# Optimization experiments

Hardware: AMD Instinct MI355X
Metric: run time of the kernel (lower is better)

## Reference

```python
import jax, jax.numpy as jnp
import numpy as np
from jax import lax

RADIUS = 4
SIGMA_1 = 5.0
SIGMA_2 = 1.0


def _gaussian_kernel_3d(radius, sigma):
    x = np.linspace(-radius, radius, 2 * radius + 1)
    xx, yy, zz = np.meshgrid(x, x, x)
    dist2 = xx ** 2 + yy ** 2 + zz ** 2
    k = np.exp(-dist2 / (2.0 * sigma ** 2)).astype(np.float32)
    return jnp.asarray(k)[None, None]  # [O=1, I=1, D, H, W]


def _conv3d_same(x, kernel, radius):
    # x: [B,1,D,H,W], kernel: [1,1,kd,kh,kw]
    pad = [(radius, radius)] * 3
    return lax.conv_general_dilated(
        x, kernel, window_strides=(1, 1, 1), padding=pad,
        dimension_numbers=('NCDHW', 'OIDHW', 'NCDHW'))


def setup_inputs() -> dict:
    key = jax.random.key(0)
    k1, k2 = jax.random.split(key)
    labels = jax.random.uniform(k1, (4, 1, 160, 160, 160), dtype=jnp.float32)
    inputs = jax.random.uniform(k2, (4, 1, 160, 160, 160), dtype=jnp.float32)
    return {"labels": labels, "inputs": inputs}


def reference(labels, inputs):
    kernel = _gaussian_kernel_3d(RADIUS, SIGMA_1)
    num_classes = 2
    p0 = labels[:, 0:1]  # [B,1,D,H,W]
    loss = jnp.float32(0.0)
    for k in range(num_classes):
        class_probs = p0 if k == 0 else 1.0 - p0
        class_mean = (jnp.mean(inputs * class_probs, axis=(2, 3, 4), keepdims=True)
                      / (jnp.mean(class_probs, axis=(2, 3, 4), keepdims=True) + 1e-5))
        diff = jnp.sum((inputs - class_mean) ** 2, axis=1, keepdims=True)  # [B,1,D,H,W]
        weights = jnp.exp(-(diff ** 2) / (SIGMA_2 ** 2))
        numerator = jnp.sum(class_probs * _conv3d_same(class_probs * weights, kernel, RADIUS))
        denominator = jnp.sum(class_probs * _conv3d_same(weights, kernel, RADIUS))
        # L1Loss(scalar, 0) == abs(scalar)
        loss = loss + jnp.abs(numerator / (denominator + 1e-6))
    return jnp.float32(num_classes) - loss
```

## Files before the change

### kernel.cpp

```cpp
#include <hip/hip_runtime.h>
#include <math.h>

#define NX   160
#define N2   25600
#define N3   4096000
#define NB   4

#define NTILES_XY 16000
#define TILES_PER_B 4000
#define NBLK_Z 800

#define SA_W 52
#define SB_W 36

__device__ __constant__ float G1[9] = {
    0.72614903f, 0.83527021f, 0.92311635f, 0.98019867f, 1.0f,
    0.98019867f, 0.92311635f, 0.83527021f, 0.72614903f};

#define ES_FULL 7.92946852f
__device__ __constant__ float ES_M[4] = {3.46473426f, 2.48453559f, 1.56141924f,
                                         0.72614903f};
__device__ inline float edge_sum(int i) {
    float s = ES_FULL;
    if (i < 4) s -= ES_M[i];
    if (i > NX - 5) s -= ES_M[NX - 1 - i];
    return s;
}

__device__ inline float4 f4_zero() { return make_float4(0.f, 0.f, 0.f, 0.f); }
__device__ inline float4 f4_axpy(float a, float4 b, float4 c) {
    return make_float4(c.x + a * b.x, c.y + a * b.y, c.z + a * b.z, c.w + a * b.w);
}

template <int NV>
__device__ inline void block_reduce_store(double* vals, double* dst) {
    __shared__ double red[4][NV];
    int lane = threadIdx.x & 63;
    int wave = threadIdx.x >> 6;
#pragma unroll
    for (int v = 0; v < NV; ++v) {
        double x = vals[v];
#pragma unroll
        for (int off = 32; off > 0; off >>= 1) x += __shfl_down(x, off, 64);
        if (lane == 0) red[wave][v] = x;
    }
    __syncthreads();
    if (threadIdx.x < NV) {
        int v = threadIdx.x;
        dst[v] = red[0][v] + red[1][v] + red[2][v] + red[3][v];
    }
}

__global__ __launch_bounds__(256) void conv_xy_kernel(
    const float* __restrict__ labels, const float* __restrict__ inputs,
    float* __restrict__ t, double* __restrict__ pS) {
    __shared__ float sA[40 * SA_W];
    __shared__ float sB[40 * SB_W];

    int bid = blockIdx.x;
    int tileX = bid % 5;
    int tileY = (bid / 5) % 5;
    int zb = bid / 25;
    int sliceOff = zb * N2;
    int x0 = tileX * 32, y0 = tileY * 32;
    int tid = threadIdx.x;

    for (int i = tid; i < 480; i += 256) {
        int row = i / 12, c = i % 12;
        int gx = x0 - 8 + 4 * c;
        int gy = y0 - 4 + row;
        float4 v = f4_zero();
        if (gy >= 0 && gy < NX && gx >= 0 && gx <= NX - 4)
            v = *(const float4*)&labels[sliceOff + gy * NX + gx];
        *(float4*)&sA[row * SA_W + 4 * c] = v;
    }
    __syncthreads();

    for (int i = tid; i < 320; i += 256) {
        int r = i >> 3, x4 = i & 7;
        const float* row = &sA[r * SA_W + 4 * x4];
        float4 a = *(const float4*)&row[4];
        float4 b = *(const float4*)&row[8];
        float4 c = *(const float4*)&row[12];
        float w[12] = {a.x, a.y, a.z, a.w, b.x, b.y, b.z, b.w,
                       c.x, c.y, c.z, c.w};
        float4 o = f4_zero();
#pragma unroll
        for (int d = 0; d < 9; ++d) {
            float g = G1[d];
            o.x += g * w[d];
            o.y += g * w[d + 1];
            o.z += g * w[d + 2];
            o.w += g * w[d + 3];
        }
        *(float4*)&sB[r * SB_W + 4 * x4] = o;
    }
    __syncthreads();

    int oy = tid >> 3, x4 = tid & 7;
    float4 acc = f4_zero();
#pragma unroll
    for (int d = 0; d < 9; ++d) {
        float4 v = *(const float4*)&sB[(oy + d) * SB_W + 4 * x4];
        acc = f4_axpy(G1[d], v, acc);
    }
    int gi = sliceOff + (y0 + oy) * NX + (x0 + 4 * x4);
    *(float4*)&t[gi] = acc;

    float4 p = *(const float4*)&sA[(oy + 4) * SA_W + 4 * x4 + 8];
    float4 in = *(const float4*)&inputs[gi];
    float sp = p.x + p.y + p.z + p.w;
    float sip = in.x * p.x + in.y * p.y + in.z * p.z + in.w * p.w;
    float si = in.x + in.y + in.z + in.w;
    double vals[3] = {(double)sp, (double)sip, (double)si};
    block_reduce_store<3>(vals, pS + 3 * bid);
}

__global__ __launch_bounds__(256) void reduce_S_kernel(
    const double* __restrict__ pS, double* __restrict__ S) {
    int b = blockIdx.x;
    double v0 = 0, v1 = 0, v2 = 0;
    for (int i = threadIdx.x; i < TILES_PER_B; i += 256) {
        const double* p = pS + 3 * (b * TILES_PER_B + i);
        v0 += p[0]; v1 += p[1]; v2 += p[2];
    }
    double vals[3] = {v0, v1, v2};
    block_reduce_store<3>(vals, S + 3 * b);
}

__global__ __launch_bounds__(256) void conv_z_reduce_kernel(
    const float* __restrict__ t, const float* __restrict__ labels,
    const float* __restrict__ inputs, const double* __restrict__ S,
    double* __restrict__ pZ) {
    int tidg = blockIdx.x * 256 + threadIdx.x;
    int x4 = tidg % 40;
    int r = tidg / 40;
    int y = r % NX;
    r /= NX;
    int zc = r % 8;
    int b = r / 8;

    double sp = S[3 * b + 0], sip = S[3 * b + 1], si = S[3 * b + 2];
    const double Nv = (double)N3;
    float m0 = (float)((sip / Nv) / (sp / Nv + 1e-5));
    float m1 = (float)(((si - sip) / Nv) / ((Nv - sp) / Nv + 1e-5));

    int x = x4 * 4;
    float ey = edge_sum(y);
    float cx[4] = {edge_sum(x) * ey, edge_sum(x + 1) * ey,
                   edge_sum(x + 2) * ey, edge_sum(x + 3) * ey};

    int z0 = zc * 20;
    int base = b * N3 + y * NX + x;

    float4 win[9];
#pragma unroll
    for (int d = 0; d < 9; ++d) {
        int z = z0 - 4 + d;
        win[d] = (z >= 0 && z < NX) ? *(const float4*)&t[base + z * N2]
                                    : f4_zero();
    }

    float n0 = 0.f, d0 = 0.f, n1 = 0.f, d1 = 0.f;
    for (int zb = 0; zb < 5; ++zb) {
        int z = z0 + 4 * zb;
        float4 tn[4], pv[4], iv[4];
#pragma unroll
        for (int j = 0; j < 4; ++j) {
            int zl = z + j + 5;
            tn[j] = (zl < NX) ? *(const float4*)&t[base + zl * N2] : f4_zero();
            int gi = base + (z + j) * N2;
            pv[j] = *(const float4*)&labels[gi];
            iv[j] = *(const float4*)&inputs[gi];
        }
#pragma unroll
        for (int j = 0; j < 4; ++j) {
            float4 c4 = f4_zero();
#pragma unroll
            for (int d = 0; d < 9; ++d) c4 = f4_axpy(G1[d], win[d], c4);
            float ez = edge_sum(z + j);
            float pc[4] = {pv[j].x, pv[j].y, pv[j].z, pv[j].w};
            float ic[4] = {iv[j].x, iv[j].y, iv[j].z, iv[j].w};
            float cc[4] = {c4.x, c4.y, c4.z, c4.w};
#pragma unroll
            for (int l = 0; l < 4; ++l) {
                float c1 = cx[l] * ez - cc[l];
                float df0 = ic[l] - m0; df0 *= df0;
                float w0 = __expf(-df0 * df0);
                float df1 = ic[l] - m1; df1 *= df1;
                float w1 = __expf(-df1 * df1);
                n0 += cc[l] * pc[l] * w0;
                d0 += cc[l] * w0;
                n1 += c1 * (1.f - pc[l]) * w1;
                d1 += c1 * w1;
            }
#pragma unroll
            for (int d = 0; d < 8; ++d) win[d] = win[d + 1];
            win[8] = tn[j];
        }
    }
    double vals[4] = {(double)n0, (double)d0, (double)n1, (double)d1};
    block_reduce_store<4>(vals, pZ + 4 * blockIdx.x);
}

__global__ __launch_bounds__(256) void finalize_kernel(
    const double* __restrict__ pZ, float* __restrict__ out) {
    double a0 = 0, a1 = 0, a2 = 0, a3 = 0;
    for (int i = threadIdx.x; i < NBLK_Z; i += 256) {
        const double* p = pZ + 4 * i;
        a0 += p[0]; a1 += p[1]; a2 += p[2]; a3 += p[3];
    }
    __shared__ double red[4][4];
    int lane = threadIdx.x & 63;
    int wave = threadIdx.x >> 6;
    double vals[4] = {a0, a1, a2, a3};
#pragma unroll
    for (int v = 0; v < 4; ++v) {
        double x = vals[v];
#pragma unroll
        for (int off = 32; off > 0; off >>= 1) x += __shfl_down(x, off, 64);
        if (lane == 0) red[wave][v] = x;
    }
    __syncthreads();
    if (threadIdx.x == 0) {
        double acc[4];
#pragma unroll
        for (int v = 0; v < 4; ++v)
            acc[v] = red[0][v] + red[1][v] + red[2][v] + red[3][v];
        double r0 = fabs(acc[0] / (acc[1] + 1e-6));
        double r1 = fabs(acc[2] / (acc[3] + 1e-6));
        out[0] = (float)(2.0 - r0 - r1);
    }
}

extern "C" void kernel_launch(void* const* d_in, const int* in_sizes, int n_in,
                              void* d_out, int out_size, void* d_ws, size_t ws_size,
                              hipStream_t stream) {
    const float* labels = (const float*)d_in[0];
    const float* inputs = (const float*)d_in[1];
    float* out = (float*)d_out;

    double* pS = (double*)d_ws;
    double* S  = (double*)((char*)d_ws + 384000);
    double* pZ = (double*)((char*)d_ws + 384096);
    float*  t  = (float*)((char*)d_ws + 524288);

    hipLaunchKernelGGL(conv_xy_kernel, dim3(NTILES_XY), dim3(256), 0, stream,
                       labels, inputs, t, pS);
    hipLaunchKernelGGL(reduce_S_kernel, dim3(NB), dim3(256), 0, stream, pS, S);
    hipLaunchKernelGGL(conv_z_reduce_kernel, dim3(NBLK_Z), dim3(256), 0, stream,
                       t, labels, inputs, S, pZ);
    hipLaunchKernelGGL(finalize_kernel, dim3(1), dim3(256), 0, stream, pZ, out);
}
```

Before: 206.4 us.

## Store XY-convolved intermediate in fp16 and fold reductions into last-block tickets

The intermediate XY-convolution buffer t is now written and read as fp16, halving its write and read traffic. The two small reduction kernels (per-batch sums and final scalar) are folded into their producers using an atomic ticket counter, so the last-finishing block does the final reduction, with counters cleared by a memset. The shared-memory staging of labels is removed in favour of direct global loads. The cost is fp16 rounding of the convolved values and an extra memset launch.

```diff
diff --git a/kernel.cpp b/kernel.cpp
--- a/kernel.cpp
+++ b/kernel.cpp
@@ -1,4 +1,5 @@
 #include <hip/hip_runtime.h>
+#include <hip/hip_fp16.h>
 #include <math.h>
 
 #define NX   160
@@ -10,7 +11,6 @@
 #define TILES_PER_B 4000
 #define NBLK_Z 800
 
-#define SA_W 52
 #define SB_W 36
 
 __device__ __constant__ float G1[9] = {
@@ -32,8 +32,17 @@
     return make_float4(c.x + a * b.x, c.y + a * b.y, c.z + a * b.z, c.w + a * b.w);
 }
 
+__device__ inline float4 load_t4(const __half* p) {
+    uint2 u = *(const uint2*)p;
+    __half2 a = *(const __half2*)&u.x;
+    __half2 b = *(const __half2*)&u.y;
+    float2 fa = __half22float2(a);
+    float2 fb = __half22float2(b);
+    return make_float4(fa.x, fa.y, fb.x, fb.y);
+}
+
 template <int NV>
-__device__ inline void block_reduce_store(double* vals, double* dst) {
+__device__ inline void block_reduce_to_t0(double* vals) {
     __shared__ double red[4][NV];
     int lane = threadIdx.x & 63;
     int wave = threadIdx.x >> 6;
@@ -45,16 +54,18 @@
         if (lane == 0) red[wave][v] = x;
     }
     __syncthreads();
-    if (threadIdx.x < NV) {
-        int v = threadIdx.x;
-        dst[v] = red[0][v] + red[1][v] + red[2][v] + red[3][v];
-    }
+    if (threadIdx.x == 0) {
+#pragma unroll
+        for (int v = 0; v < NV; ++v)
+            vals[v] = red[0][v] + red[1][v] + red[2][v] + red[3][v];
+    }
+    __syncthreads();
 }
 
 __global__ __launch_bounds__(256) void conv_xy_kernel(
     const float* __restrict__ labels, const float* __restrict__ inputs,
-    float* __restrict__ t, double* __restrict__ pS) {
-    __shared__ float sA[40 * SA_W];
+    __half* __restrict__ t, double* __restrict__ pS, double* __restrict__ S,
+    int* __restrict__ cnt) {
     __shared__ float sB[40 * SB_W];
 
     int bid = blockIdx.x;
@@ -65,25 +76,25 @@
     int x0 = tileX * 32, y0 = tileY * 32;
     int tid = threadIdx.x;
 
-    for (int i = tid; i < 480; i += 256) {
-        int row = i / 12, c = i % 12;
-        int gx = x0 - 8 + 4 * c;
-        int gy = y0 - 4 + row;
-        float4 v = f4_zero();
-        if (gy >= 0 && gy < NX && gx >= 0 && gx <= NX - 4)
-            v = *(const float4*)&labels[sliceOff + gy * NX + gx];
-        *(float4*)&sA[row * SA_W + 4 * c] = v;
-    }
-    __syncthreads();
-
     for (int i = tid; i < 320; i += 256) {
         int r = i >> 3, x4 = i & 7;
-        const float* row = &sA[r * SA_W + 4 * x4];
-        float4 a = *(const float4*)&row[4];
-        float4 b = *(const float4*)&row[8];
-        float4 c = *(const float4*)&row[12];
-        float w[12] = {a.x, a.y, a.z, a.w, b.x, b.y, b.z, b.w,
-                       c.x, c.y, c.z, c.w};
+        int gy = y0 + r - 4;
+        int gxf = x0 + 4 * x4 - 4;
+        float w[12];
+        if (gy >= 0 && gy < NX) {
+            const float* row = &labels[sliceOff + gy * NX];
+#pragma unroll
+            for (int c = 0; c < 3; ++c) {
+                int gx = gxf + 4 * c;
+                float4 v = (gx >= 0 && gx <= NX - 4) ? *(const float4*)&row[gx]
+                                                     : f4_zero();
+                w[4 * c] = v.x; w[4 * c + 1] = v.y;
+                w[4 * c + 2] = v.z; w[4 * c + 3] = v.w;
+            }
+        } else {
+#pragma unroll
+            for (int c = 0; c < 12; ++c) w[c] = 0.f;
+        }
         float4 o = f4_zero();
 #pragma unroll
         for (int d = 0; d < 9; ++d) {
@@ -105,34 +116,56 @@
         acc = f4_axpy(G1[d], v, acc);
     }
     int gi = sliceOff + (y0 + oy) * NX + (x0 + 4 * x4);
-    *(float4*)&t[gi] = acc;
-
-    float4 p = *(const float4*)&sA[(oy + 4) * SA_W + 4 * x4 + 8];
+    __half2 ha = __floats2half2_rn(acc.x, acc.y);
+    __half2 hb = __floats2half2_rn(acc.z, acc.w);
+    uint2 u;
+    u.x = *(unsigned int*)&ha;
+    u.y = *(unsigned int*)&hb;
+    *(uint2*)&t[gi] = u;
+
+    float4 p = *(const float4*)&labels[gi];
     float4 in = *(const float4*)&inputs[gi];
-    float sp = p.x + p.y + p.z + p.w;
-    float sip = in.x * p.x + in.y * p.y + in.z * p.z + in.w * p.w;
-    float si = in.x + in.y + in.z + in.w;
-    double vals[3] = {(double)sp, (double)sip, (double)si};
-    block_reduce_store<3>(vals, pS + 3 * bid);
-}
-
-__global__ __launch_bounds__(256) void reduce_S_kernel(
-    const double* __restrict__ pS, double* __restrict__ S) {
-    int b = blockIdx.x;
-    double v0 = 0, v1 = 0, v2 = 0;
-    for (int i = threadIdx.x; i < TILES_PER_B; i += 256) {
-        const double* p = pS + 3 * (b * TILES_PER_B + i);
-        v0 += p[0]; v1 += p[1]; v2 += p[2];
-    }
-    double vals[3] = {v0, v1, v2};
-    block_reduce_store<3>(vals, S + 3 * b);
-}
-
-__global__ __launch_bounds__(256) void conv_z_reduce_kernel(
-    const float* __restrict__ t, const float* __restrict__ labels,
+    double vals[3];
+    vals[0] = (double)(p.x + p.y + p.z + p.w);
+    vals[1] = (double)(in.x * p.x + in.y * p.y + in.z * p.z + in.w * p.w);
+    vals[2] = (double)(in.x + in.y + in.z + in.w);
+    block_reduce_to_t0<3>(vals);
+
+    __shared__ int lastFlag;
+    if (tid == 0) {
+        pS[bid * 3 + 0] = vals[0];
+        pS[bid * 3 + 1] = vals[1];
+        pS[bid * 3 + 2] = vals[2];
+        __threadfence();
+        int ticket = atomicAdd(cnt, 1);
+        lastFlag = (ticket == NTILES_XY - 1);
+    }
+    __syncthreads();
+    if (lastFlag) {
+        __threadfence();
+        for (int b = 0; b < NB; ++b) {
+            double a0 = 0, a1 = 0, a2 = 0;
+            for (int i = tid; i < TILES_PER_B; i += 256) {
+                const double* p2 = &pS[(b * TILES_PER_B + i) * 3];
+                a0 += p2[0]; a1 += p2[1]; a2 += p2[2];
+            }
+            double v[3] = {a0, a1, a2};
+            block_reduce_to_t0<3>(v);
+            if (tid == 0) {
+                S[3 * b + 0] = v[0];
+                S[3 * b + 1] = v[1];
+                S[3 * b + 2] = v[2];
+            }
+        }
+    }
+}
+
+__global__ __launch_bounds__(256) void conv_z_kernel(
+    const __half* __restrict__ t, const float* __restrict__ labels,
     const float* __restrict__ inputs, const double* __restrict__ S,
-    double* __restrict__ pZ) {
-    int tidg = blockIdx.x * 256 + threadIdx.x;
+    double* __restrict__ pZ, float* __restrict__ out, int* __restrict__ cnt) {
+    int tid = threadIdx.x;
+    int tidg = blockIdx.x * 256 + tid;
     int x4 = tidg % 40;
     int r = tidg / 40;
     int y = r % NX;
@@ -157,18 +190,17 @@
 #pragma unroll
     for (int d = 0; d < 9; ++d) {
         int z = z0 - 4 + d;
-        win[d] = (z >= 0 && z < NX) ? *(const float4*)&t[base + z * N2]
-                                    : f4_zero();
+        win[d] = (z >= 0 && z < NX) ? load_t4(&t[base + z * N2]) : f4_zero();
     }
 
     float n0 = 0.f, d0 = 0.f, n1 = 0.f, d1 = 0.f;
-    for (int zb = 0; zb < 5; ++zb) {
-        int z = z0 + 4 * zb;
+    for (int zb5 = 0; zb5 < 5; ++zb5) {
+        int z = z0 + 4 * zb5;
         float4 tn[4], pv[4], iv[4];
 #pragma unroll
         for (int j = 0; j < 4; ++j) {
             int zl = z + j + 5;
-            tn[j] = (zl < NX) ? *(const float4*)&t[base + zl * N2] : f4_zero();
+            tn[j] = (zl < NX) ? load_t4(&t[base + zl * N2]) : f4_zero();
             int gi = base + (z + j) * N2;
             pv[j] = *(const float4*)&labels[gi];
             iv[j] = *(const float4*)&inputs[gi];
@@ -200,36 +232,33 @@
         }
     }
     double vals[4] = {(double)n0, (double)d0, (double)n1, (double)d1};
-    block_reduce_store<4>(vals, pZ + 4 * blockIdx.x);
-}
-
-__global__ __launch_bounds__(256) void finalize_kernel(
-    const double* __restrict__ pZ, float* __restrict__ out) {
-    double a0 = 0, a1 = 0, a2 = 0, a3 = 0;
-    for (int i = threadIdx.x; i < NBLK_Z; i += 256) {
-        const double* p = pZ + 4 * i;
-        a0 += p[0]; a1 += p[1]; a2 += p[2]; a3 += p[3];
-    }
-    __shared__ double red[4][4];
-    int lane = threadIdx.x & 63;
-    int wave = threadIdx.x >> 6;
-    double vals[4] = {a0, a1, a2, a3};
-#pragma unroll
-    for (int v = 0; v < 4; ++v) {
-        double x = vals[v];
-#pragma unroll
-        for (int off = 32; off > 0; off >>= 1) x += __shfl_down(x, off, 64);
-        if (lane == 0) red[wave][v] = x;
-    }
-    __syncthreads();
-    if (threadIdx.x == 0) {
-        double acc[4];
-#pragma unroll
-        for (int v = 0; v < 4; ++v)
-            acc[v] = red[0][v] + red[1][v] + red[2][v] + red[3][v];
-        double r0 = fabs(acc[0] / (acc[1] + 1e-6));
-        double r1 = fabs(acc[2] / (acc[3] + 1e-6));
-        out[0] = (float)(2.0 - r0 - r1);
+    block_reduce_to_t0<4>(vals);
+
+    __shared__ int lastFlag;
+    if (tid == 0) {
+        pZ[blockIdx.x * 4 + 0] = vals[0];
+        pZ[blockIdx.x * 4 + 1] = vals[1];
+        pZ[blockIdx.x * 4 + 2] = vals[2];
+        pZ[blockIdx.x * 4 + 3] = vals[3];
+        __threadfence();
+        int ticket = atomicAdd(cnt, 1);
+        lastFlag = (ticket == NBLK_Z - 1);
+    }
+    __syncthreads();
+    if (lastFlag) {
+        __threadfence();
+        double a0 = 0, a1 = 0, a2 = 0, a3 = 0;
+        for (int i = tid; i < NBLK_Z; i += 256) {
+            const double* p = &pZ[4 * i];
+            a0 += p[0]; a1 += p[1]; a2 += p[2]; a3 += p[3];
+        }
+        double v[4] = {a0, a1, a2, a3};
+        block_reduce_to_t0<4>(v);
+        if (tid == 0) {
+            double r0 = fabs(v[0] / (v[1] + 1e-6));
+            double r1 = fabs(v[2] / (v[3] + 1e-6));
+            out[0] = (float)(2.0 - r0 - r1);
+        }
     }
 }
 
@@ -240,15 +269,15 @@
     const float* inputs = (const float*)d_in[1];
     float* out = (float*)d_out;
 
-    double* pS = (double*)d_ws;
-    double* S  = (double*)((char*)d_ws + 384000);
-    double* pZ = (double*)((char*)d_ws + 384096);
-    float*  t  = (float*)((char*)d_ws + 524288);
-
+    int*    cnt = (int*)d_ws;
+    double* pS  = (double*)((char*)d_ws + 256);
+    double* S   = (double*)((char*)d_ws + 384256);
+    double* pZ  = (double*)((char*)d_ws + 384384);
+    __half* t   = (__half*)((char*)d_ws + 524288);
+
+    hipMemsetAsync(cnt, 0, 8, stream);
     hipLaunchKernelGGL(conv_xy_kernel, dim3(NTILES_XY), dim3(256), 0, stream,
-                       labels, inputs, t, pS);
-    hipLaunchKernelGGL(reduce_S_kernel, dim3(NB), dim3(256), 0, stream, pS, S);
-    hipLaunchKernelGGL(conv_z_reduce_kernel, dim3(NBLK_Z), dim3(256), 0, stream,
-                       t, labels, inputs, S, pZ);
-    hipLaunchKernelGGL(finalize_kernel, dim3(1), dim3(256), 0, stream, pZ, out);
-}
+                       labels, inputs, t, pS, S, cnt);
+    hipLaunchKernelGGL(conv_z_kernel, dim3(NBLK_Z), dim3(256), 0, stream,
+                       t, labels, inputs, S, pZ, out, cnt + 1);
+}
```

New measurement: 795.7 us. 286% more time.

## Store XY-blurred intermediate in fp16 and process four z-slices per block

Applied to the files above, without the earlier changes.

The intermediate XY-convolved volume t is now written and read as half precision, halving its round-trip traffic between the two conv kernels. The XY kernel handles four z-slices per block and loads labels directly from global memory instead of staging a padded tile in shared memory. Block count and the partial-sum array shrink to match. The fp16 storage adds rounding error to the smoothed values feeding the loss ratios.

```diff
diff --git a/kernel.cpp b/kernel.cpp
--- a/kernel.cpp
+++ b/kernel.cpp
@@ -1,4 +1,5 @@
 #include <hip/hip_runtime.h>
+#include <hip/hip_fp16.h>
 #include <math.h>
 
 #define NX   160
@@ -6,12 +7,13 @@
 #define N3   4096000
 #define NB   4
 
-#define NTILES_XY 16000
-#define TILES_PER_B 4000
+#define ZPB  4
+#define NBLK_XY 4000
+#define BLKS_PER_B 1000
 #define NBLK_Z 800
 
-#define SA_W 52
 #define SB_W 36
+#define SB_PLANE (40 * SB_W)
 
 __device__ __constant__ float G1[9] = {
     0.72614903f, 0.83527021f, 0.92311635f, 0.98019867f, 1.0f,
@@ -32,6 +34,15 @@
     return make_float4(c.x + a * b.x, c.y + a * b.y, c.z + a * b.z, c.w + a * b.w);
 }
 
+__device__ inline float4 load_t4(const __half* p) {
+    uint2 u = *(const uint2*)p;
+    __half2 a = *(const __half2*)&u.x;
+    __half2 b = *(const __half2*)&u.y;
+    float2 fa = __half22float2(a);
+    float2 fb = __half22float2(b);
+    return make_float4(fa.x, fa.y, fb.x, fb.y);
+}
+
 template <int NV>
 __device__ inline void block_reduce_store(double* vals, double* dst) {
     __shared__ double red[4][NV];
@@ -53,37 +64,40 @@
 
 __global__ __launch_bounds__(256) void conv_xy_kernel(
     const float* __restrict__ labels, const float* __restrict__ inputs,
-    float* __restrict__ t, double* __restrict__ pS) {
-    __shared__ float sA[40 * SA_W];
-    __shared__ float sB[40 * SB_W];
+    __half* __restrict__ t, double* __restrict__ pS) {
+    __shared__ float sB[ZPB * SB_PLANE];
 
     int bid = blockIdx.x;
     int tileX = bid % 5;
     int tileY = (bid / 5) % 5;
-    int zb = bid / 25;
-    int sliceOff = zb * N2;
+    int zq = (bid / 25) % 40;
+    int b = bid / BLKS_PER_B;
+    int zbase = zq * ZPB;
     int x0 = tileX * 32, y0 = tileY * 32;
     int tid = threadIdx.x;
-
-    for (int i = tid; i < 480; i += 256) {
-        int row = i / 12, c = i % 12;
-        int gx = x0 - 8 + 4 * c;
-        int gy = y0 - 4 + row;
-        float4 v = f4_zero();
-        if (gy >= 0 && gy < NX && gx >= 0 && gx <= NX - 4)
-            v = *(const float4*)&labels[sliceOff + gy * NX + gx];
-        *(float4*)&sA[row * SA_W + 4 * c] = v;
-    }
-    __syncthreads();
-
-    for (int i = tid; i < 320; i += 256) {
-        int r = i >> 3, x4 = i & 7;
-        const float* row = &sA[r * SA_W + 4 * x4];
-        float4 a = *(const float4*)&row[4];
-        float4 b = *(const float4*)&row[8];
-        float4 c = *(const float4*)&row[12];
-        float w[12] = {a.x, a.y, a.z, a.w, b.x, b.y, b.z, b.w,
-                       c.x, c.y, c.z, c.w};
+    int baseOff = b * N3 + zbase * N2;
+
+    for (int i = tid; i < ZPB * 320; i += 256) {
+        int j = i / 320;
+        int rem = i - 320 * j;
+        int r = rem >> 3, x4 = rem & 7;
+        int gy = y0 + r - 4;
+        int gxf = x0 + 4 * x4 - 4;
+        float w[12];
+        if (gy >= 0 && gy < NX) {
+            const float* row = &labels[baseOff + j * N2 + gy * NX];
+#pragma unroll
+            for (int c = 0; c < 3; ++c) {
+                int gx = gxf + 4 * c;
+                float4 v = (gx >= 0 && gx <= NX - 4) ? *(const float4*)&row[gx]
+                                                     : f4_zero();
+                w[4 * c] = v.x; w[4 * c + 1] = v.y;
+                w[4 * c + 2] = v.z; w[4 * c + 3] = v.w;
+            }
+        } else {
+#pragma unroll
+            for (int c = 0; c < 12; ++c) w[c] = 0.f;
+        }
         float4 o = f4_zero();
 #pragma unroll
         for (int d = 0; d < 9; ++d) {
@@ -93,26 +107,35 @@
             o.z += g * w[d + 2];
             o.w += g * w[d + 3];
         }
-        *(float4*)&sB[r * SB_W + 4 * x4] = o;
+        *(float4*)&sB[j * SB_PLANE + r * SB_W + 4 * x4] = o;
     }
     __syncthreads();
 
     int oy = tid >> 3, x4 = tid & 7;
-    float4 acc = f4_zero();
-#pragma unroll
-    for (int d = 0; d < 9; ++d) {
-        float4 v = *(const float4*)&sB[(oy + d) * SB_W + 4 * x4];
-        acc = f4_axpy(G1[d], v, acc);
-    }
-    int gi = sliceOff + (y0 + oy) * NX + (x0 + 4 * x4);
-    *(float4*)&t[gi] = acc;
-
-    float4 p = *(const float4*)&sA[(oy + 4) * SA_W + 4 * x4 + 8];
-    float4 in = *(const float4*)&inputs[gi];
-    float sp = p.x + p.y + p.z + p.w;
-    float sip = in.x * p.x + in.y * p.y + in.z * p.z + in.w * p.w;
-    float si = in.x + in.y + in.z + in.w;
-    double vals[3] = {(double)sp, (double)sip, (double)si};
+    double sp = 0.0, sip = 0.0, si = 0.0;
+#pragma unroll
+    for (int j = 0; j < ZPB; ++j) {
+        float4 acc = f4_zero();
+#pragma unroll
+        for (int d = 0; d < 9; ++d) {
+            float4 v = *(const float4*)&sB[j * SB_PLANE + (oy + d) * SB_W + 4 * x4];
+            acc = f4_axpy(G1[d], v, acc);
+        }
+        int gi = baseOff + j * N2 + (y0 + oy) * NX + (x0 + 4 * x4);
+        __half2 ha = __floats2half2_rn(acc.x, acc.y);
+        __half2 hb = __floats2half2_rn(acc.z, acc.w);
+        uint2 u;
+        u.x = *(unsigned int*)&ha;
+        u.y = *(unsigned int*)&hb;
+        *(uint2*)&t[gi] = u;
+
+        float4 p = *(const float4*)&labels[gi];
+        float4 in = *(const float4*)&inputs[gi];
+        sp += (double)(p.x + p.y + p.z + p.w);
+        sip += (double)(in.x * p.x + in.y * p.y + in.z * p.z + in.w * p.w);
+        si += (double)(in.x + in.y + in.z + in.w);
+    }
+    double vals[3] = {sp, sip, si};
     block_reduce_store<3>(vals, pS + 3 * bid);
 }
 
@@ -120,19 +143,20 @@
     const double* __restrict__ pS, double* __restrict__ S) {
     int b = blockIdx.x;
     double v0 = 0, v1 = 0, v2 = 0;
-    for (int i = threadIdx.x; i < TILES_PER_B; i += 256) {
-        const double* p = pS + 3 * (b * TILES_PER_B + i);
+    for (int i = threadIdx.x; i < BLKS_PER_B; i += 256) {
+        const double* p = pS + 3 * (b * BLKS_PER_B + i);
         v0 += p[0]; v1 += p[1]; v2 += p[2];
     }
     double vals[3] = {v0, v1, v2};
     block_reduce_store<3>(vals, S + 3 * b);
 }
 
-__global__ __launch_bounds__(256) void conv_z_reduce_kernel(
-    const float* __restrict__ t, const float* __restrict__ labels,
+__global__ __launch_bounds__(256) void conv_z_kernel(
+    const __half* __restrict__ t, const float* __restrict__ labels,
     const float* __restrict__ inputs, const double* __restrict__ S,
     double* __restrict__ pZ) {
-    int tidg = blockIdx.x * 256 + threadIdx.x;
+    int tid = threadIdx.x;
+    int tidg = blockIdx.x * 256 + tid;
     int x4 = tidg % 40;
     int r = tidg / 40;
     int y = r % NX;
@@ -157,18 +181,17 @@
 #pragma unroll
     for (int d = 0; d < 9; ++d) {
         int z = z0 - 4 + d;
-        win[d] = (z >= 0 && z < NX) ? *(const float4*)&t[base + z * N2]
-                                    : f4_zero();
+        win[d] = (z >= 0 && z < NX) ? load_t4(&t[base + z * N2]) : f4_zero();
     }
 
     float n0 = 0.f, d0 = 0.f, n1 = 0.f, d1 = 0.f;
-    for (int zb = 0; zb < 5; ++zb) {
-        int z = z0 + 4 * zb;
+    for (int zb5 = 0; zb5 < 5; ++zb5) {
+        int z = z0 + 4 * zb5;
         float4 tn[4], pv[4], iv[4];
 #pragma unroll
         for (int j = 0; j < 4; ++j) {
             int zl = z + j + 5;
-            tn[j] = (zl < NX) ? *(const float4*)&t[base + zl * N2] : f4_zero();
+            tn[j] = (zl < NX) ? load_t4(&t[base + zl * N2]) : f4_zero();
             int gi = base + (z + j) * N2;
             pv[j] = *(const float4*)&labels[gi];
             iv[j] = *(const float4*)&inputs[gi];
@@ -207,7 +230,7 @@
     const double* __restrict__ pZ, float* __restrict__ out) {
     double a0 = 0, a1 = 0, a2 = 0, a3 = 0;
     for (int i = threadIdx.x; i < NBLK_Z; i += 256) {
-        const double* p = pZ + 4 * i;
+        const double* p = &pZ[4 * i];
         a0 += p[0]; a1 += p[1]; a2 += p[2]; a3 += p[3];
     }
     __shared__ double red[4][4];
@@ -241,14 +264,14 @@
     float* out = (float*)d_out;
 
     double* pS = (double*)d_ws;
-    double* S  = (double*)((char*)d_ws + 384000);
-    double* pZ = (double*)((char*)d_ws + 384096);
-    float*  t  = (float*)((char*)d_ws + 524288);
-
-    hipLaunchKernelGGL(conv_xy_kernel, dim3(NTILES_XY), dim3(256), 0, stream,
+    double* S  = (double*)((char*)d_ws + 96000);
+    double* pZ = (double*)((char*)d_ws + 96128);
+    __half* t  = (__half*)((char*)d_ws + 524288);
+
+    hipLaunchKernelGGL(conv_xy_kernel, dim3(NBLK_XY), dim3(256), 0, stream,
                        labels, inputs, t, pS);
     hipLaunchKernelGGL(reduce_S_kernel, dim3(NB), dim3(256), 0, stream, pS, S);
-    hipLaunchKernelGGL(conv_z_reduce_kernel, dim3(NBLK_Z), dim3(256), 0, stream,
+    hipLaunchKernelGGL(conv_z_kernel, dim3(NBLK_Z), dim3(256), 0, stream,
                        t, labels, inputs, S, pZ);
     hipLaunchKernelGGL(finalize_kernel, dim3(1), dim3(256), 0, stream, pZ, out);
 }
```

After: 198.7 us. 1.04x faster.

## Store xy-convolved intermediate in fp16, fold S reduction into z kernel, split z finer

Applied to the files above, without the earlier changes.

The intermediate xy-convolved field is now written and read as fp16, halving its traffic through memory. The separate per-batch reduce kernel is removed and each z-pass block redundantly reduces its batch's 4000 partial sums itself. The z range per thread shrinks from 20 to 10 slices, doubling the block count for more parallelism. The cost is fp16 rounding of the convolution result, a redundant 12k-double read per block, and a larger relative halo overhead in z.

```diff
diff --git a/kernel.cpp b/kernel.cpp
--- a/kernel.cpp
+++ b/kernel.cpp
@@ -1,4 +1,5 @@
 #include <hip/hip_runtime.h>
+#include <hip/hip_fp16.h>
 #include <math.h>
 
 #define NX   160
@@ -6,9 +7,10 @@
 #define N3   4096000
 #define NB   4
 
-#define NTILES_XY 16000
+#define NBLK_XY 16000
 #define TILES_PER_B 4000
-#define NBLK_Z 800
+#define NBLK_Z 1600
+#define ZCH 10
 
 #define SA_W 52
 #define SB_W 36
@@ -32,6 +34,15 @@
     return make_float4(c.x + a * b.x, c.y + a * b.y, c.z + a * b.z, c.w + a * b.w);
 }
 
+__device__ inline float4 load_t4(const __half* p) {
+    uint2 u = *(const uint2*)p;
+    __half2 a = *(const __half2*)&u.x;
+    __half2 b = *(const __half2*)&u.y;
+    float2 fa = __half22float2(a);
+    float2 fb = __half22float2(b);
+    return make_float4(fa.x, fa.y, fb.x, fb.y);
+}
+
 template <int NV>
 __device__ inline void block_reduce_store(double* vals, double* dst) {
     __shared__ double red[4][NV];
@@ -53,7 +64,7 @@
 
 __global__ __launch_bounds__(256) void conv_xy_kernel(
     const float* __restrict__ labels, const float* __restrict__ inputs,
-    float* __restrict__ t, double* __restrict__ pS) {
+    __half* __restrict__ t, double* __restrict__ pS) {
     __shared__ float sA[40 * SA_W];
     __shared__ float sB[40 * SB_W];
 
@@ -105,42 +116,46 @@
         acc = f4_axpy(G1[d], v, acc);
     }
     int gi = sliceOff + (y0 + oy) * NX + (x0 + 4 * x4);
-    *(float4*)&t[gi] = acc;
+    __half2 ha = __floats2half2_rn(acc.x, acc.y);
+    __half2 hb = __floats2half2_rn(acc.z, acc.w);
+    uint2 u;
+    u.x = *(unsigned int*)&ha;
+    u.y = *(unsigned int*)&hb;
+    *(uint2*)&t[gi] = u;
 
     float4 p = *(const float4*)&sA[(oy + 4) * SA_W + 4 * x4 + 8];
     float4 in = *(const float4*)&inputs[gi];
-    float sp = p.x + p.y + p.z + p.w;
-    float sip = in.x * p.x + in.y * p.y + in.z * p.z + in.w * p.w;
-    float si = in.x + in.y + in.z + in.w;
-    double vals[3] = {(double)sp, (double)sip, (double)si};
+    double vals[3];
+    vals[0] = (double)(p.x + p.y + p.z + p.w);
+    vals[1] = (double)(in.x * p.x + in.y * p.y + in.z * p.z + in.w * p.w);
+    vals[2] = (double)(in.x + in.y + in.z + in.w);
     block_reduce_store<3>(vals, pS + 3 * bid);
 }
 
-__global__ __launch_bounds__(256) void reduce_S_kernel(
-    const double* __restrict__ pS, double* __restrict__ S) {
-    int b = blockIdx.x;
-    double v0 = 0, v1 = 0, v2 = 0;
-    for (int i = threadIdx.x; i < TILES_PER_B; i += 256) {
-        const double* p = pS + 3 * (b * TILES_PER_B + i);
-        v0 += p[0]; v1 += p[1]; v2 += p[2];
-    }
-    double vals[3] = {v0, v1, v2};
-    block_reduce_store<3>(vals, S + 3 * b);
-}
-
-__global__ __launch_bounds__(256) void conv_z_reduce_kernel(
-    const float* __restrict__ t, const float* __restrict__ labels,
-    const float* __restrict__ inputs, const double* __restrict__ S,
+__global__ __launch_bounds__(256) void conv_z_kernel(
+    const __half* __restrict__ t, const float* __restrict__ labels,
+    const float* __restrict__ inputs, const double* __restrict__ pS,
     double* __restrict__ pZ) {
-    int tidg = blockIdx.x * 256 + threadIdx.x;
+    int tid = threadIdx.x;
+    int tidg = blockIdx.x * 256 + tid;
     int x4 = tidg % 40;
     int r = tidg / 40;
     int y = r % NX;
-    r /= NX;
-    int zc = r % 8;
-    int b = r / 8;
-
-    double sp = S[3 * b + 0], sip = S[3 * b + 1], si = S[3 * b + 2];
+    int zc = (tidg / 6400) % 16;
+    int b = tidg / 102400;
+
+    __shared__ double Ssh[3];
+    {
+        double v0 = 0, v1 = 0, v2 = 0;
+        for (int i = tid; i < TILES_PER_B; i += 256) {
+            const double* p = pS + 3 * (b * TILES_PER_B + i);
+            v0 += p[0]; v1 += p[1]; v2 += p[2];
+        }
+        double vals[3] = {v0, v1, v2};
+        block_reduce_store<3>(vals, Ssh);
+        __syncthreads();
+    }
+    double sp = Ssh[0], sip = Ssh[1], si = Ssh[2];
     const double Nv = (double)N3;
     float m0 = (float)((sip / Nv) / (sp / Nv + 1e-5));
     float m1 = (float)(((si - sip) / Nv) / ((Nv - sp) / Nv + 1e-5));
@@ -150,35 +165,35 @@
     float cx[4] = {edge_sum(x) * ey, edge_sum(x + 1) * ey,
                    edge_sum(x + 2) * ey, edge_sum(x + 3) * ey};
 
-    int z0 = zc * 20;
+    int z0 = zc * ZCH;
     int base = b * N3 + y * NX + x;
 
     float4 win[9];
 #pragma unroll
     for (int d = 0; d < 9; ++d) {
         int z = z0 - 4 + d;
-        win[d] = (z >= 0 && z < NX) ? *(const float4*)&t[base + z * N2]
-                                    : f4_zero();
+        win[d] = (z >= 0 && z < NX) ? load_t4(&t[base + z * N2]) : f4_zero();
     }
 
     float n0 = 0.f, d0 = 0.f, n1 = 0.f, d1 = 0.f;
-    for (int zb = 0; zb < 5; ++zb) {
-        int z = z0 + 4 * zb;
-        float4 tn[4], pv[4], iv[4];
-#pragma unroll
-        for (int j = 0; j < 4; ++j) {
-            int zl = z + j + 5;
-            tn[j] = (zl < NX) ? *(const float4*)&t[base + zl * N2] : f4_zero();
-            int gi = base + (z + j) * N2;
+#pragma unroll
+    for (int g = 0; g < 2; ++g) {
+        int zg = z0 + 5 * g;
+        float4 tn[5], pv[5], iv[5];
+#pragma unroll
+        for (int j = 0; j < 5; ++j) {
+            int zl = zg + j + 5;
+            tn[j] = (zl < NX) ? load_t4(&t[base + zl * N2]) : f4_zero();
+            int gi = base + (zg + j) * N2;
             pv[j] = *(const float4*)&labels[gi];
             iv[j] = *(const float4*)&inputs[gi];
         }
 #pragma unroll
-        for (int j = 0; j < 4; ++j) {
+        for (int j = 0; j < 5; ++j) {
             float4 c4 = f4_zero();
 #pragma unroll
             for (int d = 0; d < 9; ++d) c4 = f4_axpy(G1[d], win[d], c4);
-            float ez = edge_sum(z + j);
+            float ez = edge_sum(zg + j);
             float pc[4] = {pv[j].x, pv[j].y, pv[j].z, pv[j].w};
             float ic[4] = {iv[j].x, iv[j].y, iv[j].z, iv[j].w};
             float cc[4] = {c4.x, c4.y, c4.z, c4.w};
@@ -207,7 +222,7 @@
     const double* __restrict__ pZ, float* __restrict__ out) {
     double a0 = 0, a1 = 0, a2 = 0, a3 = 0;
     for (int i = threadIdx.x; i < NBLK_Z; i += 256) {
-        const double* p = pZ + 4 * i;
+        const double* p = &pZ[4 * i];
         a0 += p[0]; a1 += p[1]; a2 += p[2]; a3 += p[3];
     }
     __shared__ double red[4][4];
@@ -241,14 +256,12 @@
     float* out = (float*)d_out;
 
     double* pS = (double*)d_ws;
-    double* S  = (double*)((char*)d_ws + 384000);
-    double* pZ = (double*)((char*)d_ws + 384096);
-    float*  t  = (float*)((char*)d_ws + 524288);
-
-    hipLaunchKernelGGL(conv_xy_kernel, dim3(NTILES_XY), dim3(256), 0, stream,
+    double* pZ = (double*)((char*)d_ws + 384000);
+    __half* t  = (__half*)((char*)d_ws + 524288);
+
+    hipLaunchKernelGGL(conv_xy_kernel, dim3(NBLK_XY), dim3(256), 0, stream,
                        labels, inputs, t, pS);
-    hipLaunchKernelGGL(reduce_S_kernel, dim3(NB), dim3(256), 0, stream, pS, S);
-    hipLaunchKernelGGL(conv_z_reduce_kernel, dim3(NBLK_Z), dim3(256), 0, stream,
-                       t, labels, inputs, S, pZ);
+    hipLaunchKernelGGL(conv_z_kernel, dim3(NBLK_Z), dim3(256), 0, stream,
+                       t, labels, inputs, pS, pZ);
     hipLaunchKernelGGL(finalize_kernel, dim3(1), dim3(256), 0, stream, pZ, out);
 }
```

New measurement: 227.0 us. 1.1x slower.
